# Performance work log

Measured on AMD Instinct MI355X. Metric: run time of the kernel, lower is better.

Reference implementation:

```python
import jax, jax.numpy as jnp
import numpy as np

HID = 1024      # hidden_size (embedding dim, GRU input)
RNN = 1024      # rnn_hidden_size
VOCAB = 50000   # max_node
STEPS = 1024    # num_steps
SOS = 0


def setup_inputs() -> dict:
    key = jax.random.key(0)
    ks = jax.random.split(key, 8)
    s = 0.02
    return {
        "inputs": jax.random.randint(ks[0], (STEPS,), 0, VOCAB),
        "z": jax.random.normal(ks[1], (RNN,), jnp.float32),
        "emb_W": jax.random.uniform(ks[2], (VOCAB, HID), jnp.float32, -0.001, 0.001),
        "out_b": jnp.full((VOCAB,), 0.01, jnp.float32),
        "h2e_W": jax.random.normal(ks[3], (HID, RNN), jnp.float32) * s,
        "h2e_b": jnp.full((HID,), 0.01, jnp.float32),
        "W_ih": jax.random.normal(ks[4], (3 * RNN, HID), jnp.float32) * s,
        "W_hh": jax.random.normal(ks[5], (3 * RNN, RNN), jnp.float32) * s,
        "b_ih": jnp.zeros((3 * RNN,), jnp.float32),
        "b_hh": jnp.zeros((3 * RNN,), jnp.float32),
    }


def reference(inputs, z, emb_W, out_b, h2e_W, h2e_b, W_ih, W_hh, b_ih, b_hh):
    R = RNN

    def gru_cell(h, x):
        gi = W_ih @ x + b_ih          # (3R,)
        gh = W_hh @ h + b_hh          # (3R,)
        r = jax.nn.sigmoid(gi[:R] + gh[:R])
        zg = jax.nn.sigmoid(gi[R:2 * R] + gh[R:2 * R])
        n = jnp.tanh(gi[2 * R:] + r * gh[2 * R:])
        return (1.0 - zg) * n + zg * h

    # teacher forcing: step i consumes token_{i-1} (SOS for i=1), target is inputs[i]
    step_tokens = jnp.concatenate([jnp.array([SOS], dtype=inputs.dtype), inputs[1:-1]])
    targets = inputs[1:]

    def step(h, tok_tgt):
        tok, tgt = tok_tgt
        x = emb_W[tok]                              # embedding lookup (HID,)
        h_new = gru_cell(h, x)                      # (RNN,)
        e = h2e_W @ h_new + h2e_b                   # (HID,)
        logp = jax.nn.log_softmax(emb_W @ e + out_b)  # tied weights, (VOCAB,)
        return h_new, (-logp[tgt], jnp.argmax(logp))

    _, (losses, preds) = jax.lax.scan(step, z, (step_tokens, targets))
    loss = jnp.sum(losses)
    outputs = jnp.zeros((1, inputs.shape[0]), dtype=jnp.int32).at[0, 1:].set(preds.astype(jnp.int32))
    return loss, outputs
```

## Files before the change

### kernel.cpp

```cpp
#include <hip/hip_runtime.h>
#include <math.h>

#define NV      50000
#define T_STEPS 1023
#define KDIM    1024
typedef unsigned long long ull;

#define NRECUR  64
#define NEW_    16
#define NLW     147
#define NBLK    (NRECUR + NEW_ + NLW)
#define ERING   512
#define NSTRIPE 49
#define NBATCH  64
#define BSTEP   16
#define TSB     24576
#define CANDI_OFF 6272
#define NCAND   1568


__global__ __launch_bounds__(256) void k_gather(const int* __restrict__ inputs,
                                                const float* __restrict__ emb,
                                                float* __restrict__ X) {
  const int t = blockIdx.x;
  const int tid = threadIdx.x;
  float4 v = make_float4(0.f, 0.f, 0.f, 0.f);
  if (t < T_STEPS) {
    const int tok = (t == 0) ? 0 : inputs[t];
    v = *(const float4*)&emb[(size_t)tok * KDIM + tid * 4];
  }
  *(float4*)&X[(size_t)t * KDIM + tid * 4] = v;
}

__global__ __launch_bounds__(256) void k_gemm_ffd(const float* __restrict__ A,
                                                  const float* __restrict__ B,
                                                  const float* __restrict__ bias,
                                                  double* __restrict__ C,
                                                  int N, int K) {
  __shared__ float As[32][68];
  __shared__ float Bs[32][68];
  const int tid = threadIdx.x;
  const int bx = blockIdx.x, by = blockIdx.y;
  const int lr = tid >> 2;
  const int lk = (tid & 3) * 8;
  const float* Ap = A + (size_t)(by * 64 + lr) * K + lk;
  const float* Bp = B + (size_t)(bx * 64 + lr) * K + lk;
  const int r0 = (tid >> 4) * 4;
  const int c0 = (tid & 15) * 4;
  double acc[4][4] = {};
  for (int kc = 0; kc < K; kc += 32) {
    const float4 a0 = *(const float4*)(Ap + kc);
    const float4 a1 = *(const float4*)(Ap + kc + 4);
    const float4 b0 = *(const float4*)(Bp + kc);
    const float4 b1 = *(const float4*)(Bp + kc + 4);
    __syncthreads();
    As[lk+0][lr]=a0.x; As[lk+1][lr]=a0.y; As[lk+2][lr]=a0.z; As[lk+3][lr]=a0.w;
    As[lk+4][lr]=a1.x; As[lk+5][lr]=a1.y; As[lk+6][lr]=a1.z; As[lk+7][lr]=a1.w;
    Bs[lk+0][lr]=b0.x; Bs[lk+1][lr]=b0.y; Bs[lk+2][lr]=b0.z; Bs[lk+3][lr]=b0.w;
    Bs[lk+4][lr]=b1.x; Bs[lk+5][lr]=b1.y; Bs[lk+6][lr]=b1.z; Bs[lk+7][lr]=b1.w;
    __syncthreads();
#pragma unroll
    for (int kk = 0; kk < 32; ++kk) {
      const float4 av = *(const float4*)&As[kk][r0];
      const float4 bv = *(const float4*)&Bs[kk][c0];
      const double aa[4] = {av.x, av.y, av.z, av.w};
      const double bb[4] = {bv.x, bv.y, bv.z, bv.w};
#pragma unroll
      for (int i = 0; i < 4; ++i)
#pragma unroll
        for (int j = 0; j < 4; ++j)
          acc[i][j] = fma(aa[i], bb[j], acc[i][j]);
    }
  }
  const int row = by * 64 + r0;
  const int col = bx * 64 + c0;
#pragma unroll
  for (int i = 0; i < 4; ++i)
#pragma unroll
    for (int j = 0; j < 4; ++j)
      C[(size_t)(row + i) * N + col + j] = acc[i][j] + (double)bias[col + j];
}

__global__ __launch_bounds__(512, 1) void k_mega(
    const float* z, const float* Whh, const float* bhh,
    const double* GI, double* H, ull* SA, ull* SB, int* done,
    int* prog, int* Edone, int* bcount, double* Ering,
    const float* h2eW, const float* h2eb,
    const float* emb, const float* out_b, const int* inputs,
    float* Psum, float* Ttgt, char* candb)
{
  __shared__ double SM[2048];
  const int tid = threadIdx.x;
  const int bid = blockIdx.x;

  if (bid < NRECUR) {
    double* hs = SM;
    const int w = tid >> 6, l = tid & 63;
    const int ibase = bid * 16 + w * 2;
    float wreg[6][16];
#pragma unroll
    for (int il = 0; il < 2; ++il)
#pragma unroll
      for (int g = 0; g < 3; ++g) {
        const float* wp = Whh + (size_t)(g * 1024 + ibase + il) * 1024 + l;
#pragma unroll
        for (int m = 0; m < 16; ++m) wreg[il * 3 + g][m] = wp[m * 64];
      }
    double bh[6];
#pragma unroll
    for (int il = 0; il < 2; ++il)
#pragma unroll
      for (int g = 0; g < 3; ++g) bh[il * 3 + g] = (double)bhh[g * 1024 + ibase + il];

    hs[tid]       = (double)z[tid];
    hs[tid + 512] = (double)z[tid + 512];
    double gi[6];
#pragma unroll
    for (int il = 0; il < 2; ++il)
#pragma unroll
      for (int g = 0; g < 3; ++g) gi[il * 3 + g] = GI[g * 1024 + ibase + il];
    __syncthreads();

    for (int t = 0; t < T_STEPS; ++t) {
      const bool more = (t + 1 < T_STEPS);
      const int p = t & 1;
      const bool gate = more && (t >= 2);
      int dv = 0x7FFFFFFF;
      if (gate && tid < 64)
        dv = __hip_atomic_load(done + p * 64 + tid,
                               __ATOMIC_RELAXED, __HIP_MEMORY_SCOPE_AGENT);
      double s[6] = {0.0, 0.0, 0.0, 0.0, 0.0, 0.0};
#pragma unroll
      for (int m = 0; m < 16; ++m) {
        const double hv = hs[l + 64 * m];
#pragma unroll
        for (int rr = 0; rr < 6; ++rr) s[rr] = fma((double)wreg[rr][m], hv, s[rr]);
      }
#pragma unroll
      for (int rr = 0; rr < 6; ++rr) {
        double v = s[rr];
#pragma unroll
        for (int mk = 32; mk >= 1; mk >>= 1) v += __shfl_xor(v, mk, 64);
        s[rr] = v;
      }
      double hn = 0.0;
      if (l < 2) {
        const int il = l;
        const double r  = 1.0 / (1.0 + exp(-(gi[il*3+0] + s[il*3+0] + bh[il*3+0])));
        const double zg = 1.0 / (1.0 + exp(-(gi[il*3+1] + s[il*3+1] + bh[il*3+1])));
        const double n  = tanh(gi[il*3+2] + r * (s[il*3+2] + bh[il*3+2]));
        hn = (1.0 - zg) * n + zg * hs[ibase + l];
      }
      double gin[6] = {0.0, 0.0, 0.0, 0.0, 0.0, 0.0};
      if (more) {
        const double* gp = GI + (size_t)(t + 1) * 3072;
#pragma unroll
        for (int il = 0; il < 2; ++il)
#pragma unroll
          for (int g = 0; g < 3; ++g) gin[il * 3 + g] = gp[g * 1024 + ibase + il];
      }
      if (gate && tid < 64) {
        while (!__all(dv >= t - 1)) {
          __builtin_amdgcn_s_sleep(1);
          dv = __hip_atomic_load(done + p * 64 + tid,
                                 __ATOMIC_RELAXED, __HIP_MEMORY_SCOPE_AGENT);
        }
      }
      __syncthreads();
      if (l < 2) {
        const int gidx = ibase + l;
        __hip_atomic_store(H + (size_t)t * 1024 + gidx, hn,
                           __ATOMIC_RELAXED, __HIP_MEMORY_SCOPE_AGENT);
        if (more) {
          const ull hb  = (ull)__double_as_longlong(hn);
          const ull tag = ((ull)(t + 1)) << 32;
          __hip_atomic_store(SA + p * 1024 + gidx, tag | (hb >> 32),
                             __ATOMIC_RELAXED, __HIP_MEMORY_SCOPE_AGENT);
          __hip_atomic_store(SB + p * 1024 + gidx, tag | (hb & 0xFFFFFFFFull),
                             __ATOMIC_RELAXED, __HIP_MEMORY_SCOPE_AGENT);
        }
      }
      if (more) {
        const ull want = (ull)(t + 1);
        ull a0, b0, a1, b1;
        while (true) {
          a0 = __hip_atomic_load(SA + p * 1024 + tid,
                                 __ATOMIC_RELAXED, __HIP_MEMORY_SCOPE_AGENT);
          b0 = __hip_atomic_load(SB + p * 1024 + tid,
                                 __ATOMIC_RELAXED, __HIP_MEMORY_SCOPE_AGENT);
          if ((a0 >> 32) >= want && (b0 >> 32) >= want) break;
          __builtin_amdgcn_s_sleep(1);
        }
        while (true) {
          a1 = __hip_atomic_load(SA + p * 1024 + tid + 512,
                                 __ATOMIC_RELAXED, __HIP_MEMORY_SCOPE_AGENT);
          b1 = __hip_atomic_load(SB + p * 1024 + tid + 512,
                                 __ATOMIC_RELAXED, __HIP_MEMORY_SCOPE_AGENT);
          if ((a1 >> 32) >= want && (b1 >> 32) >= want) break;
          __builtin_amdgcn_s_sleep(1);
        }
        hs[tid]       = __longlong_as_double((long long)
                          (((a0 & 0xFFFFFFFFull) << 32) | (b0 & 0xFFFFFFFFull)));
        hs[tid + 512] = __longlong_as_double((long long)
                          (((a1 & 0xFFFFFFFFull) << 32) | (b1 & 0xFFFFFFFFull)));
        __syncthreads();
        if (tid == 0) {
          __hip_atomic_store(done + p * 64 + bid, t + 1,
                             __ATOMIC_RELAXED, __HIP_MEMORY_SCOPE_AGENT);
          __hip_atomic_store(prog + bid, t + 1,
                             __ATOMIC_RELAXED, __HIP_MEMORY_SCOPE_AGENT);
        }
#pragma unroll
        for (int q = 0; q < 6; ++q) gi[q] = gin[q];
      }
    }
    __syncthreads();
    if (tid == 0)
      __hip_atomic_store(prog + bid, T_STEPS,
                         __ATOMIC_RELAXED, __HIP_MEMORY_SCOPE_AGENT);

  } else if (bid < NRECUR + NEW_) {
    const int e = bid - NRECUR;
    for (int s = e; s < T_STEPS; s += NEW_) {
      if (s >= ERING && tid == 0) {
        const int bi = (s - ERING) >> 4;
        while (__hip_atomic_load(bcount + bi, __ATOMIC_RELAXED,
                                 __HIP_MEMORY_SCOPE_AGENT) < NSTRIPE)
          __builtin_amdgcn_s_sleep(8);
      }
      if (tid < 64) {
        while (true) {
          const int pv = __hip_atomic_load(prog + tid, __ATOMIC_RELAXED,
                                           __HIP_MEMORY_SCOPE_AGENT);
          if (__all(pv >= s + 1)) break;
          __builtin_amdgcn_s_sleep(8);
        }
      }
      __syncthreads();
      SM[tid]       = __hip_atomic_load(H + (size_t)s * 1024 + tid,
                        __ATOMIC_RELAXED, __HIP_MEMORY_SCOPE_AGENT);
      SM[tid + 512] = __hip_atomic_load(H + (size_t)s * 1024 + tid + 512,
                        __ATOMIC_RELAXED, __HIP_MEMORY_SCOPE_AGENT);
      __syncthreads();
      double a0 = 0.0, a1 = 0.0;
      const float* w0 = h2eW + (size_t)tid * 1024;
      const float* w1 = h2eW + (size_t)(tid + 512) * 1024;
      for (int k = 0; k < 1024; ++k) {
        const double hv = SM[k];
        a0 = fma((double)w0[k], hv, a0);
        a1 = fma((double)w1[k], hv, a1);
      }
      double* er = Ering + (size_t)(s & (ERING - 1)) * 1024;
      __hip_atomic_store(er + tid, a0 + (double)h2eb[tid],
                         __ATOMIC_RELAXED, __HIP_MEMORY_SCOPE_AGENT);
      __hip_atomic_store(er + tid + 512, a1 + (double)h2eb[tid + 512],
                         __ATOMIC_RELAXED, __HIP_MEMORY_SCOPE_AGENT);
      __syncthreads();
      if (tid == 0)
        __hip_atomic_store(Edone + s, 1,
                           __ATOMIC_RELAXED, __HIP_MEMORY_SCOPE_AGENT);
    }

  } else {
    const int wk = bid - NRECUR - NEW_;
    const int wv = tid >> 6, lane = tid & 63;
    for (int u = wk; u < NBATCH * NSTRIPE; u += NLW) {
      const int b = u / NSTRIPE, j = u - b * NSTRIPE;
      const int s0 = b * BSTEP;
      if (tid < 64) {
        while (true) {
          const int ss = s0 + lane;
          const int ev = (lane < BSTEP && ss < T_STEPS)
              ? __hip_atomic_load(Edone + ss, __ATOMIC_RELAXED,
                                  __HIP_MEMORY_SCOPE_AGENT) : 1;
          if (__all(ev != 0)) break;
          __builtin_amdgcn_s_sleep(8);
        }
      }
      const int cbase = j * 1024 + wv * 128;
      const int col0 = cbase + lane, col1 = cbase + 64 + lane;
      const bool cv0 = col0 < NV, cv1 = col1 < NV;
      const float* e0p = emb + (size_t)(cv0 ? col0 : 0) * 1024;
      const float* e1p = emb + (size_t)(cv1 ? col1 : 0) * 1024;
      const float ob0 = cv0 ? out_b[col0] : 0.f;
      const float ob1 = cv1 ? out_b[col1] : 0.f;
      double acc0[BSTEP] = {}, acc1[BSTEP] = {};
      for (int kt = 0; kt < 8; ++kt) {
        const int kb = kt * 128;
        __syncthreads();
        for (int li = tid; li < 2048; li += 512) {
          const int si = li & 15, kj = li >> 4;
          SM[li] = __hip_atomic_load(
              Ering + (size_t)((s0 + si) & (ERING - 1)) * 1024 + kb + kj,
              __ATOMIC_RELAXED, __HIP_MEMORY_SCOPE_AGENT);
        }
        __syncthreads();
#pragma unroll 2
        for (int kj = 0; kj < 128; kj += 4) {
          const float4 f0 = *(const float4*)(e0p + kb + kj);
          const float4 f1 = *(const float4*)(e1p + kb + kj);
          const float b0a[4] = {f0.x, f0.y, f0.z, f0.w};
          const float b1a[4] = {f1.x, f1.y, f1.z, f1.w};
#pragma unroll
          for (int q = 0; q < 4; ++q) {
            const double* ev = &SM[(kj + q) * 16];
            const double d0 = (double)b0a[q], d1 = (double)b1a[q];
#pragma unroll
            for (int si = 0; si < BSTEP; ++si) {
              acc0[si] = fma(ev[si], d0, acc0[si]);
              acc1[si] = fma(ev[si], d1, acc1[si]);
            }
          }
        }
      }
      float* clbase;
      int*   cibase;
#pragma unroll
      for (int si = 0; si < BSTEP; ++si) {
        const int s = s0 + si;
        if (s < T_STEPS) {
          const int tgt = inputs[s + 1];
          const double lgd0 = acc0[si] + (double)ob0;
          const double lgd1 = acc1[si] + (double)ob1;
          float L1a = cv0 ? (float)lgd0 : -3e38f;
          int   i1a = cv0 ? col0 : 0x7FFFFFFF;
          float L2a = -3e38f; int i2a = 0x7FFFFFFF;
          float L1b = cv1 ? (float)lgd1 : -3e38f;
          int   i1b = cv1 ? col1 : 0x7FFFFFFF;
          float L2b = -3e38f; int i2b = 0x7FFFFFFF;
          float se = (cv0 ? expf((float)(lgd0 - 0.01)) : 0.f)
                   + (cv1 ? expf((float)(lgd1 - 0.01)) : 0.f);
          float tv = -INFINITY;
          if (cv0 && col0 == tgt) tv = (float)lgd0;
          if (cv1 && col1 == tgt) tv = (float)lgd1;
#pragma unroll
          for (int mk = 1; mk <= 32; mk <<= 1) {
            const float oL1a = __shfl_xor(L1a, mk, 64);
            const int   oi1a = __shfl_xor(i1a, mk, 64);
            const float oL2a = __shfl_xor(L2a, mk, 64);
            const int   oi2a = __shfl_xor(i2a, mk, 64);
            if (oL1a > L1a || (oL1a == L1a && oi1a < i1a)) { L2a = L1a; i2a = i1a; L1a = oL1a; i1a = oi1a; }
            else if (oL1a > L2a || (oL1a == L2a && oi1a < i2a)) { L2a = oL1a; i2a = oi1a; }
            if (oL2a > L1a || (oL2a == L1a && oi2a < i1a)) { L2a = L1a; i2a = i1a; L1a = oL2a; i1a = oi2a; }
            else if (oL2a > L2a || (oL2a == L2a && oi2a < i2a)) { L2a = oL2a; i2a = oi2a; }
            const float oL1b = __shfl_xor(L1b, mk, 64);
            const int   oi1b = __shfl_xor(i1b, mk, 64);
            const float oL2b = __shfl_xor(L2b, mk, 64);
            const int   oi2b = __shfl_xor(i2b, mk, 64);
            if (oL1b > L1b || (oL1b == L1b && oi1b < i1b)) { L2b = L1b; i2b = i1b; L1b = oL1b; i1b = oi1b; }
            else if (oL1b > L2b || (oL1b == L2b && oi1b < i2b)) { L2b = oL1b; i2b = oi1b; }
            if (oL2b > L1b || (oL2b == L1b && oi2b < i1b)) { L2b = L1b; i2b = i1b; L1b = oL2b; i1b = oi2b; }
            else if (oL2b > L2b || (oL2b == L2b && oi2b < i2b)) { L2b = oL2b; i2b = oi2b; }
            se += __shfl_xor(se, mk, 64);
            tv = fmaxf(tv, __shfl_xor(tv, mk, 64));
          }
          if (lane == 0) {
            clbase = (float*)(candb + (size_t)s * TSB);
            cibase = (int*)(candb + (size_t)s * TSB + CANDI_OFF);
            const int c0 = j * 16 + wv * 2;
            clbase[c0 * 2]     = L1a;  cibase[c0 * 2]     = i1a;
            clbase[c0 * 2 + 1] = L2a;  cibase[c0 * 2 + 1] = i2a;
            clbase[c0 * 2 + 2] = L1b;  cibase[c0 * 2 + 2] = i1b;
            clbase[c0 * 2 + 3] = L2b;  cibase[c0 * 2 + 3] = i2b;
            atomicAdd(Psum + s, se);
            if (tv > -1e30f) Ttgt[s] = tv;
          }
        }
      }
      __syncthreads();
      if (tid == 0) atomicAdd(bcount + b, 1);
    }
  }
}

__global__ __launch_bounds__(256) void k_preds(const char* __restrict__ candb,
                                               float* __restrict__ out) {
  __shared__ float sL[256];
  __shared__ int   sI[256];
  const int s = blockIdx.x;
  const int tid = threadIdx.x;
  const float* candL = (const float*)(candb + (size_t)s * TSB);
  const int*   candI = (const int*)(candb + (size_t)s * TSB + CANDI_OFF);
  const int n = NCAND;
  float m = -3e38f;
  for (int c = tid; c < n; c += 256) m = fmaxf(m, candL[c]);
  sL[tid] = m; __syncthreads();
  for (int st = 128; st > 0; st >>= 1) {
    if (tid < st) sL[tid] = fmaxf(sL[tid], sL[tid + st]);
    __syncthreads();
  }
  const float Lmax = sL[0];
  __syncthreads();
  float bq = -3e38f; int bi = 0x7FFFFFFF;
  for (int c = tid; c < n; c += 256) {
    const float L = candL[c];
    const int   v = candI[c];
    const float d = L - Lmax;
    const float q = d - 10.8125f;
    if (q > bq || (q == bq && v < bi)) { bq = q; bi = v; }
  }
  sL[tid] = bq; sI[tid] = bi; __syncthreads();
  for (int st = 128; st > 0; st >>= 1) {
    if (tid < st) {
      if (sL[tid + st] > sL[tid] ||
          (sL[tid + st] == sL[tid] && sI[tid + st] < sI[tid])) {
        sL[tid] = sL[tid + st]; sI[tid] = sI[tid + st];
      }
    }
    __syncthreads();
  }
  if (tid == 0) out[2 + s] = (float)sI[0];
}

__global__ __launch_bounds__(1024) void k_finish(const float* __restrict__ Psum,
                                                 const float* __restrict__ Ttgt,
                                                 float* __restrict__ out) {
  __shared__ double red[1024];
  const int s = threadIdx.x;
  double ls = 0.0;
  if (s < T_STEPS) ls = 0.01 + log((double)Psum[s]) - (double)Ttgt[s];
  red[s] = ls;
  __syncthreads();
  for (int st = 512; st > 0; st >>= 1) {
    if (s < st) red[s] += red[s + st];
    __syncthreads();
  }
  if (s == 0) out[0] = (float)red[0];
  if (s == 1) out[1] = 0.f;
}

extern "C" void kernel_launch(void* const* d_in, const int* in_sizes, int n_in,
                              void* d_out, int out_size, void* d_ws, size_t ws_size,
                              hipStream_t stream) {
  const int*   inputs = (const int*)  d_in[0];
  const float* z      = (const float*)d_in[1];
  const float* emb    = (const float*)d_in[2];
  const float* out_b  = (const float*)d_in[3];
  const float* h2eW   = (const float*)d_in[4];
  const float* h2eb   = (const float*)d_in[5];
  const float* Wih    = (const float*)d_in[6];
  const float* Whh    = (const float*)d_in[7];
  const float* bih    = (const float*)d_in[8];
  const float* bhh    = (const float*)d_in[9];

  char* ws8 = (char*)d_ws;
  ull*    SA     = (ull*)ws8;
  ull*    SB     = (ull*)(ws8 + 16384);
  int*    done   = (int*)(ws8 + 32768);
  int*    prog   = (int*)(ws8 + 33280);
  int*    Edone  = (int*)(ws8 + 33536);
  int*    bcount = (int*)(ws8 + 37632);
  float*  Psum   = (float*)(ws8 + 40960);
  float*  Ttgt   = (float*)(ws8 + 45056);
  char*   GIb    = ws8 + 98304;
  double* GI     = (double*)GIb;
  double* XE     = (double*)(GIb + (24u << 20));
  double* H      = (double*)(GIb + (28u << 20));
  float*  out    = (float*)d_out;

  hipMemsetAsync(ws8, 0, 49152, stream);

  k_gather<<<1024, 256, 0, stream>>>(inputs, emb, (float*)XE);
  k_gemm_ffd<<<dim3(48, 16), 256, 0, stream>>>((float*)XE, Wih, bih, GI,
                                               3072, KDIM);
  k_mega<<<NBLK, 512, 0, stream>>>(z, Whh, bhh, GI, H, SA, SB, done,
                                   prog, Edone, bcount, XE, h2eW, h2eb,
                                   emb, out_b, inputs, Psum, Ttgt, GIb);
  k_preds<<<T_STEPS, 256, 0, stream>>>(GIb, out);
  k_finish<<<1, 1024, 0, stream>>>(Psum, Ttgt, out);
}
```

Baseline: 10.05 ms.

## Retile logits workers to 128-step batches over 128-column stripes

The logits worker tile moves from 16 steps by 1024 vocab columns to 128 steps by 128 columns. Each wave now handles 16 steps of a shared 128-step e-vector tile staged in LDS, so each embedding row read from memory is reused across 128 steps instead of 16. The cost is coarser batching: workers must wait for 128 e-vectors before starting, which lengthens pipeline fill and stalls the ring producer. Candidate slots per step grow to 1564, and the plain (non-atomic) loads of the e-ring lean on the preceding synchronization.

```diff
diff --git a/kernel.cpp b/kernel.cpp
--- a/kernel.cpp
+++ b/kernel.cpp
@@ -11,12 +11,12 @@
 #define NLW     147
 #define NBLK    (NRECUR + NEW_ + NLW)
 #define ERING   512
-#define NSTRIPE 49
-#define NBATCH  64
-#define BSTEP   16
+#define NSTRIPE 391
+#define NBATCH  8
+#define BSTEP   128
 #define TSB     24576
 #define CANDI_OFF 6272
-#define NCAND   1568
+#define NCAND   1564
 
 
 __global__ __launch_bounds__(256) void k_gather(const int* __restrict__ inputs,
@@ -89,7 +89,7 @@
     const float* emb, const float* out_b, const int* inputs,
     float* Psum, float* Ttgt, char* candb)
 {
-  __shared__ double SM[2048];
+  __shared__ double SM[4096];
   const int tid = threadIdx.x;
   const int bid = blockIdx.x;
 
@@ -223,7 +223,7 @@
     const int e = bid - NRECUR;
     for (int s = e; s < T_STEPS; s += NEW_) {
       if (s >= ERING && tid == 0) {
-        const int bi = (s - ERING) >> 4;
+        const int bi = (s - ERING) >> 7;
         while (__hip_atomic_load(bcount + bi, __ATOMIC_RELAXED,
                                  __HIP_MEMORY_SCOPE_AGENT) < NSTRIPE)
           __builtin_amdgcn_s_sleep(8);
@@ -269,55 +269,62 @@
       const int s0 = b * BSTEP;
       if (tid < 64) {
         while (true) {
-          const int ss = s0 + lane;
-          const int ev = (lane < BSTEP && ss < T_STEPS)
-              ? __hip_atomic_load(Edone + ss, __ATOMIC_RELAXED,
+          const int s1 = s0 + lane, s2 = s0 + 64 + lane;
+          const int e1 = (s1 < T_STEPS)
+              ? __hip_atomic_load(Edone + s1, __ATOMIC_RELAXED,
                                   __HIP_MEMORY_SCOPE_AGENT) : 1;
-          if (__all(ev != 0)) break;
+          const int e2 = (s2 < T_STEPS)
+              ? __hip_atomic_load(Edone + s2, __ATOMIC_RELAXED,
+                                  __HIP_MEMORY_SCOPE_AGENT) : 1;
+          if (__all((e1 != 0) && (e2 != 0))) break;
           __builtin_amdgcn_s_sleep(8);
         }
       }
-      const int cbase = j * 1024 + wv * 128;
+      const int cbase = j * 128;
       const int col0 = cbase + lane, col1 = cbase + 64 + lane;
       const bool cv0 = col0 < NV, cv1 = col1 < NV;
       const float* e0p = emb + (size_t)(cv0 ? col0 : 0) * 1024;
       const float* e1p = emb + (size_t)(cv1 ? col1 : 0) * 1024;
       const float ob0 = cv0 ? out_b[col0] : 0.f;
       const float ob1 = cv1 ? out_b[col1] : 0.f;
-      double acc0[BSTEP] = {}, acc1[BSTEP] = {};
-      for (int kt = 0; kt < 8; ++kt) {
-        const int kb = kt * 128;
+      double acc0[16] = {}, acc1[16] = {};
+      const int sstage = tid & 127, kstage = (tid >> 7) * 8;
+      const double* esrc = Ering
+          + (size_t)((s0 + sstage) & (ERING - 1)) * 1024 + kstage;
+      for (int kt = 0; kt < 32; ++kt) {
+        const int kb = kt * 32;
         __syncthreads();
-        for (int li = tid; li < 2048; li += 512) {
-          const int si = li & 15, kj = li >> 4;
-          SM[li] = __hip_atomic_load(
-              Ering + (size_t)((s0 + si) & (ERING - 1)) * 1024 + kb + kj,
-              __ATOMIC_RELAXED, __HIP_MEMORY_SCOPE_AGENT);
+        {
+          const double* sp = esrc + kb;
+#pragma unroll
+          for (int q = 0; q < 8; ++q)
+            SM[(kstage + q) * 128 + sstage] = sp[q];
         }
         __syncthreads();
 #pragma unroll 2
-        for (int kj = 0; kj < 128; kj += 4) {
+        for (int kj = 0; kj < 32; kj += 4) {
           const float4 f0 = *(const float4*)(e0p + kb + kj);
           const float4 f1 = *(const float4*)(e1p + kb + kj);
           const float b0a[4] = {f0.x, f0.y, f0.z, f0.w};
           const float b1a[4] = {f1.x, f1.y, f1.z, f1.w};
 #pragma unroll
           for (int q = 0; q < 4; ++q) {
-            const double* ev = &SM[(kj + q) * 16];
             const double d0 = (double)b0a[q], d1 = (double)b1a[q];
-#pragma unroll
-            for (int si = 0; si < BSTEP; ++si) {
-              acc0[si] = fma(ev[si], d0, acc0[si]);
-              acc1[si] = fma(ev[si], d1, acc1[si]);
+            const double* ep = SM + (size_t)(kj + q) * 128 + wv * 16;
+#pragma unroll
+            for (int sp = 0; sp < 8; ++sp) {
+              const double2 ev = *(const double2*)(ep + sp * 2);
+              acc0[sp*2]   = fma(ev.x, d0, acc0[sp*2]);
+              acc0[sp*2+1] = fma(ev.y, d0, acc0[sp*2+1]);
+              acc1[sp*2]   = fma(ev.x, d1, acc1[sp*2]);
+              acc1[sp*2+1] = fma(ev.y, d1, acc1[sp*2+1]);
             }
           }
         }
       }
-      float* clbase;
-      int*   cibase;
-#pragma unroll
-      for (int si = 0; si < BSTEP; ++si) {
-        const int s = s0 + si;
+#pragma unroll
+      for (int si = 0; si < 16; ++si) {
+        const int s = s0 + wv * 16 + si;
         if (s < T_STEPS) {
           const int tgt = inputs[s + 1];
           const double lgd0 = acc0[si] + (double)ob0;
@@ -355,13 +362,13 @@
             tv = fmaxf(tv, __shfl_xor(tv, mk, 64));
           }
           if (lane == 0) {
-            clbase = (float*)(candb + (size_t)s * TSB);
-            cibase = (int*)(candb + (size_t)s * TSB + CANDI_OFF);
-            const int c0 = j * 16 + wv * 2;
-            clbase[c0 * 2]     = L1a;  cibase[c0 * 2]     = i1a;
-            clbase[c0 * 2 + 1] = L2a;  cibase[c0 * 2 + 1] = i2a;
-            clbase[c0 * 2 + 2] = L1b;  cibase[c0 * 2 + 2] = i1b;
-            clbase[c0 * 2 + 3] = L2b;  cibase[c0 * 2 + 3] = i2b;
+            float* cl = (float*)(candb + (size_t)s * TSB);
+            int*   ci = (int*)(candb + (size_t)s * TSB + CANDI_OFF);
+            const int cha = j * 2, chb = j * 2 + 1;
+            cl[cha * 2]     = L1a;  ci[cha * 2]     = i1a;
+            cl[cha * 2 + 1] = L2a;  ci[cha * 2 + 1] = i2a;
+            cl[chb * 2]     = L1b;  ci[chb * 2]     = i1b;
+            cl[chb * 2 + 1] = L2b;  ci[chb * 2 + 1] = i2b;
             atomicAdd(Psum + s, se);
             if (tv > -1e30f) Ttgt[s] = tv;
           }
```

Result: slower. 10.43 ms (+3.8%).
